# Performance work log

Measured on AMD Instinct MI355X. Metric: run time of the kernel, lower is better.

## Reference

```python
import jax, jax.numpy as jnp
import numpy as np
from jax import lax

INPUT_DIM = 2048
OUTPUT_DIM = 2048
BATCH = 256
T = 20.0
DT = 0.5
TAU_M = 20.0
TAU_S = 5.0
STEPS = int(T / DT)  # 40


def setup_inputs() -> dict:
    key = jax.random.key(0)
    k1, k2 = jax.random.split(key)
    # spike times on the t = i*dt grid (exactly representable in fp32)
    steps_idx = jax.random.randint(k1, (BATCH, INPUT_DIM), 0, STEPS)
    inp = steps_idx.astype(jnp.float32) * DT
    # nn.init.normal_(weight, mean=0.1, std=0.1)
    weight = 0.1 + 0.1 * jax.random.normal(k2, (OUTPUT_DIM, INPUT_DIM), dtype=jnp.float32)
    return {"input": inp, "weight": weight}


def _manual_forward(inp, weight):
    B = inp.shape[0]
    O = weight.shape[0]
    V0 = jnp.zeros((B, O), dtype=weight.dtype)
    I0 = jnp.zeros((B, O), dtype=weight.dtype)  # I[-1] row is zero at i=0

    def step(carry, i):
        V, I_prev = carry
        t = i.astype(weight.dtype) * DT
        V = V + (DT / TAU_M) * (I_prev - V)
        spikes_in = (inp == t).astype(weight.dtype)            # [B, in]
        I_i = (1.0 - DT / TAU_S) * I_prev + spikes_in @ weight.T  # [B, out]
        s = (V > 1.0).astype(weight.dtype)
        V = (1.0 - s) * V
        return (V, I_i), (I_i, s)

    (_, _), (I, post_spikes) = lax.scan(step, (V0, I0), jnp.arange(STEPS))
    # first spike time: idx decreasing so argmax picks earliest spiking step
    idx = jnp.arange(STEPS, 0, -1, dtype=weight.dtype)[:, None, None]
    first = jnp.argmax(idx * post_spikes, axis=0).astype(jnp.float32)
    # neurons with no spike (or spike at step 0, faithful to original) -> T
    first = jnp.where(first == 0.0, jnp.float32(T), first)
    return first, I, post_spikes


def reference(input, weight):
    first_post_spikes, _, _ = _manual_forward(input, weight)
    return first_post_spikes
```

## Files before the change

### kernel.cpp

```cpp
#include <hip/hip_runtime.h>


#define IN_DIM     2048
#define OUT_DIM    2048
#define BATCH      256
#define STEPS      40
#define NSLICE     32
#define ORD_STRIDE 2304

__global__ __launch_bounds__(256) void transpose_k(const float* __restrict__ W,
                                                   float* __restrict__ WT) {
    __shared__ float tile[64][65];
    const int bx = blockIdx.x;
    const int by = blockIdx.y;
    const int x  = threadIdx.x & 63;
    const int y4 = threadIdx.x >> 6;
#pragma unroll
    for (int i = 0; i < 16; ++i) {
        const int a = y4 * 16 + i;
        tile[a][x] = W[(size_t)(by * 64 + a) * IN_DIM + (bx * 64 + x)];
    }
    if (bx == 0 && y4 == 0)
        WT[(size_t)IN_DIM * OUT_DIM + by * 64 + x] = 0.0f;
    __syncthreads();
#pragma unroll
    for (int i = 0; i < 16; ++i) {
        const int r = y4 * 16 + i;
        WT[(size_t)(bx * 64 + r) * OUT_DIM + (by * 64 + x)] = tile[x][r];
    }
}

__global__ __launch_bounds__(256) void sort_k(const float* __restrict__ inp,
                                              int* __restrict__ ord,
                                              int* __restrict__ offs) {
    __shared__ int hist[256 * STEPS];
    __shared__ int tot[STEPS];
    __shared__ int binstart[STEPS + 1];
    const int b = blockIdx.x, t = threadIdx.x;
    for (int i = t; i < 256 * STEPS; i += 256) hist[i] = 0;
    __syncthreads();
    int ks[8];
#pragma unroll
    for (int i = 0; i < 8; ++i) {
        const float v = inp[b * IN_DIM + t * 8 + i];
        const int k = (int)(v * 2.0f);
        ks[i] = k;
        ++hist[t * STEPS + k];
    }
    __syncthreads();
    if (t < STEPS) {
        int run = 0;
        for (int tt = 0; tt < 256; ++tt) {
            const int c = hist[tt * STEPS + t];
            hist[tt * STEPS + t] = run;
            run += c;
        }
        tot[t] = run;
    }
    __syncthreads();
    if (t == 0) {
        int run = 0;
        for (int k = 0; k < STEPS; ++k) {
            binstart[k] = run;
            run += (tot[k] + 3) & ~3;
        }
        binstart[STEPS] = run;
    }
    __syncthreads();
    if (t <= STEPS) offs[b * (STEPS + 1) + t] = binstart[t];
#pragma unroll
    for (int i = 0; i < 8; ++i) {
        const int k = ks[i];
        const int pos = binstart[k] + hist[t * STEPS + k]++;
        ord[b * ORD_STRIDE + pos] = (t * 8 + i) * (OUT_DIM * 4);
    }
    if (t < STEPS) {
        const int beg = binstart[t] + tot[t];
        const int end = binstart[t] + ((tot[t] + 3) & ~3);
        for (int p = beg; p < end; ++p)
            ord[b * ORD_STRIDE + p] = IN_DIM * (OUT_DIM * 4);
    }
}

__global__ __launch_bounds__(64) void snn_k(const float* __restrict__ WT,
                                            const int* __restrict__ ord,
                                            const int* __restrict__ offs,
                                            float* __restrict__ out) {
    const int wid  = blockIdx.x;
    const int s    = wid & (NSLICE - 1);
    const int b    = wid >> 5;
    const int lane = threadIdx.x;
    const char* wb = (const char*)(WT + s * 64 + lane);
    const int* __restrict__ ob  = ord  + b * ORD_STRIDE;
    const int* __restrict__ off = offs + b * (STEPS + 1);

    float I = 0.f, V = 0.f;
    int   f = 0;
    int p = 0;
    for (int k = 0; k < STEPS; ++k) {
        const int e = off[k + 1];
        float a = 0.f;
        for (; p < e; p += 4) {
            const int4 jj = *(const int4*)(ob + p);
            a += *(const float*)(wb + jj.x);
            a += *(const float*)(wb + jj.y);
            a += *(const float*)(wb + jj.z);
            a += *(const float*)(wb + jj.w);
        }
        V += 0.025f * (I - V);
        I = 0.9f * I + a;
        if (V > 1.0f) { if (f == 0) f = k; V = 0.f; }
        if (__all(f != 0)) break;
    }
    out[(size_t)b * OUT_DIM + s * 64 + lane] = f ? (float)f : 20.0f;
}

extern "C" void kernel_launch(void* const* d_in, const int* in_sizes, int n_in,
                              void* d_out, int out_size, void* d_ws, size_t ws_size,
                              hipStream_t stream) {
    const float* inp = (const float*)d_in[0];
    const float* W   = (const float*)d_in[1];
    float* out = (float*)d_out;
    char*  ws  = (char*)d_ws;

    float* WT = (float*)ws;
    const size_t WT_BYTES = (size_t)(IN_DIM + 1) * OUT_DIM * sizeof(float);
    int* ord  = (int*)(ws + WT_BYTES);
    int* offs = (int*)(ws + WT_BYTES + (size_t)BATCH * ORD_STRIDE * sizeof(int));

    transpose_k<<<dim3(IN_DIM / 64, OUT_DIM / 64), 256, 0, stream>>>(W, WT);
    sort_k<<<BATCH, 256, 0, stream>>>(inp, ord, offs);
    snn_k<<<BATCH * NSLICE, 64, 0, stream>>>(WT, ord, offs, out);
}
```

Baseline: 53.65 us.

## Fuse transpose and sort into one prep kernel, parallelize histogram scan

Merges the weight transpose and the per-batch counting sort into a single launch, with the first 256 blocks doing the sort and the remaining blocks doing transpose tiles, sharing one shared-memory buffer. The sort's column-wise prefix scan, previously done serially by 40 threads over 256 entries each, is split into 160 threads that each handle a quarter chunk, followed by a chunk-offset pass and an in-place scan that folds in the bin start. This removes one kernel launch and shortens the serial scan, at the cost of a larger shared-memory footprint for the transpose blocks, which may lower their occupancy, and an extra barrier in the sort path.

```diff
diff --git a/kernel.cpp b/kernel.cpp
--- a/kernel.cpp
+++ b/kernel.cpp
@@ -8,35 +8,43 @@
 #define NSLICE     32
 #define ORD_STRIDE 2304
 
-__global__ __launch_bounds__(256) void transpose_k(const float* __restrict__ W,
-                                                   float* __restrict__ WT) {
-    __shared__ float tile[64][65];
-    const int bx = blockIdx.x;
-    const int by = blockIdx.y;
-    const int x  = threadIdx.x & 63;
-    const int y4 = threadIdx.x >> 6;
-#pragma unroll
-    for (int i = 0; i < 16; ++i) {
-        const int a = y4 * 16 + i;
-        tile[a][x] = W[(size_t)(by * 64 + a) * IN_DIM + (bx * 64 + x)];
-    }
-    if (bx == 0 && y4 == 0)
-        WT[(size_t)IN_DIM * OUT_DIM + by * 64 + x] = 0.0f;
-    __syncthreads();
-#pragma unroll
-    for (int i = 0; i < 16; ++i) {
-        const int r = y4 * 16 + i;
-        WT[(size_t)(bx * 64 + r) * OUT_DIM + (by * 64 + x)] = tile[x][r];
-    }
-}
-
-__global__ __launch_bounds__(256) void sort_k(const float* __restrict__ inp,
+__global__ __launch_bounds__(256) void prep_k(const float* __restrict__ W,
+                                              float* __restrict__ WT,
+                                              const float* __restrict__ inp,
                                               int* __restrict__ ord,
                                               int* __restrict__ offs) {
-    __shared__ int hist[256 * STEPS];
-    __shared__ int tot[STEPS];
-    __shared__ int binstart[STEPS + 1];
-    const int b = blockIdx.x, t = threadIdx.x;
+    __shared__ __align__(16) char smem[43008];
+    const int t = threadIdx.x;
+
+    if (blockIdx.x >= BATCH) {
+        float (*tile)[65] = (float (*)[65])smem;
+        const int id = blockIdx.x - BATCH;
+        const int bx = id & 31;
+        const int by = id >> 5;
+        const int x  = t & 63;
+        const int y4 = t >> 6;
+#pragma unroll
+        for (int i = 0; i < 16; ++i) {
+            const int a = y4 * 16 + i;
+            tile[a][x] = W[(size_t)(by * 64 + a) * IN_DIM + (bx * 64 + x)];
+        }
+        if (bx == 0 && y4 == 0)
+            WT[(size_t)IN_DIM * OUT_DIM + by * 64 + x] = 0.0f;
+        __syncthreads();
+#pragma unroll
+        for (int i = 0; i < 16; ++i) {
+            const int r = y4 * 16 + i;
+            WT[(size_t)(bx * 64 + r) * OUT_DIM + (by * 64 + x)] = tile[x][r];
+        }
+        return;
+    }
+
+    int* hist     = (int*)smem;
+    int* chunkcnt = (int*)(smem + 40960);
+    int* binstart = (int*)(smem + 40960 + 640);
+    int* tot      = (int*)(smem + 40960 + 640 + 164);
+    const int b = blockIdx.x;
+
     for (int i = t; i < 256 * STEPS; i += 256) hist[i] = 0;
     __syncthreads();
     int ks[8];
@@ -48,30 +56,51 @@
         ++hist[t * STEPS + k];
     }
     __syncthreads();
-    if (t < STEPS) {
+    if (t < STEPS * 4) {
+        const int k = t >> 2, q = t & 3;
         int run = 0;
-        for (int tt = 0; tt < 256; ++tt) {
-            const int c = hist[tt * STEPS + t];
-            hist[tt * STEPS + t] = run;
-            run += c;
+#pragma unroll
+        for (int i = 0; i < 64; i += 8) {
+            const int base = (q * 64 + i) * STEPS + k;
+            const int c0 = hist[base + 0 * STEPS], c1 = hist[base + 1 * STEPS];
+            const int c2 = hist[base + 2 * STEPS], c3 = hist[base + 3 * STEPS];
+            const int c4 = hist[base + 4 * STEPS], c5 = hist[base + 5 * STEPS];
+            const int c6 = hist[base + 6 * STEPS], c7 = hist[base + 7 * STEPS];
+            run += ((c0 + c1) + (c2 + c3)) + ((c4 + c5) + (c6 + c7));
         }
-        tot[t] = run;
+        chunkcnt[k * 4 + q] = run;
     }
     __syncthreads();
     if (t == 0) {
         int run = 0;
         for (int k = 0; k < STEPS; ++k) {
             binstart[k] = run;
-            run += (tot[k] + 3) & ~3;
+            const int tk = (chunkcnt[k * 4] + chunkcnt[k * 4 + 1]) +
+                           (chunkcnt[k * 4 + 2] + chunkcnt[k * 4 + 3]);
+            tot[k] = tk;
+            run += (tk + 3) & ~3;
         }
         binstart[STEPS] = run;
     }
     __syncthreads();
     if (t <= STEPS) offs[b * (STEPS + 1) + t] = binstart[t];
+    if (t < STEPS * 4) {
+        const int k = t >> 2, q = t & 3;
+        int run = binstart[k];
+        for (int qq = 0; qq < q; ++qq) run += chunkcnt[k * 4 + qq];
+#pragma unroll 8
+        for (int i = 0; i < 64; ++i) {
+            const int a = (q * 64 + i) * STEPS + k;
+            const int c = hist[a];
+            hist[a] = run;
+            run += c;
+        }
+    }
+    __syncthreads();
 #pragma unroll
     for (int i = 0; i < 8; ++i) {
         const int k = ks[i];
-        const int pos = binstart[k] + hist[t * STEPS + k]++;
+        const int pos = hist[t * STEPS + k]++;
         ord[b * ORD_STRIDE + pos] = (t * 8 + i) * (OUT_DIM * 4);
     }
     if (t < STEPS) {
@@ -128,7 +157,6 @@
     int* ord  = (int*)(ws + WT_BYTES);
     int* offs = (int*)(ws + WT_BYTES + (size_t)BATCH * ORD_STRIDE * sizeof(int));
 
-    transpose_k<<<dim3(IN_DIM / 64, OUT_DIM / 64), 256, 0, stream>>>(W, WT);
-    sort_k<<<BATCH, 256, 0, stream>>>(inp, ord, offs);
+    prep_k<<<BATCH + (IN_DIM / 64) * (OUT_DIM / 64), 256, 0, stream>>>(W, WT, inp, ord, offs);
     snn_k<<<BATCH * NSLICE, 64, 0, stream>>>(WT, ord, offs, out);
 }
```

After: 45.78 us. 14.7% less time.

## Fuse per-batch spike bucketing into the SNN kernel using shared memory

Applied to the files above, without the earlier changes.

The separate sort kernel is removed. Each 256-thread block of the SNN kernel now builds the per-step bucketed spike index list for its batch row in LDS and then runs four waves over different output slices. The global ord/offs round trip and one launch go away, the accumulation loop is unrolled to 8 gathers per iteration, and the transpose grid is linearized. In exchange, each batch row's sort is redone by 8 blocks, and the blocks use more LDS, which may limit occupancy.

```diff
diff --git a/kernel.cpp b/kernel.cpp
--- a/kernel.cpp
+++ b/kernel.cpp
@@ -1,18 +1,20 @@
 #include <hip/hip_runtime.h>
 
 
-#define IN_DIM     2048
-#define OUT_DIM    2048
-#define BATCH      256
-#define STEPS      40
-#define NSLICE     32
-#define ORD_STRIDE 2304
+#define IN_DIM   2048
+#define OUT_DIM  2048
+#define BATCH    256
+#define STEPS    40
+#define ROWBYTES (OUT_DIM * 4)
+#define HS       41
+#define ORD_CAP  2176
 
 __global__ __launch_bounds__(256) void transpose_k(const float* __restrict__ W,
                                                    float* __restrict__ WT) {
     __shared__ float tile[64][65];
-    const int bx = blockIdx.x;
-    const int by = blockIdx.y;
+    const int id = blockIdx.x;
+    const int by = id & 31;
+    const int bx = id >> 5;
     const int x  = threadIdx.x & 63;
     const int y4 = threadIdx.x >> 6;
 #pragma unroll
@@ -30,82 +32,104 @@
     }
 }
 
-__global__ __launch_bounds__(256) void sort_k(const float* __restrict__ inp,
-                                              int* __restrict__ ord,
-                                              int* __restrict__ offs) {
-    __shared__ int hist[256 * STEPS];
+__global__ __launch_bounds__(256) void snn_k(const float* __restrict__ WT,
+                                             const float* __restrict__ inp,
+                                             float* __restrict__ out) {
+    __shared__ __align__(16) int ordl[ORD_CAP];
+    __shared__ int hist[64 * HS];
+    __shared__ int bs[STEPS + 1];
     __shared__ int tot[STEPS];
-    __shared__ int binstart[STEPS + 1];
-    const int b = blockIdx.x, t = threadIdx.x;
-    for (int i = t; i < 256 * STEPS; i += 256) hist[i] = 0;
+
+    const int bid = blockIdx.x;
+    const int sg  = bid & 7;
+    const int b   = bid >> 3;
+    const int t   = threadIdx.x;
+
+    for (int i = t; i < 64 * HS; i += 256) hist[i] = 0;
     __syncthreads();
-    int ks[8];
+
+    int ks[32];
+    if (t < 64) {
+        const float* row = inp + (size_t)b * IN_DIM + t * 32;
 #pragma unroll
-    for (int i = 0; i < 8; ++i) {
-        const float v = inp[b * IN_DIM + t * 8 + i];
-        const int k = (int)(v * 2.0f);
-        ks[i] = k;
-        ++hist[t * STEPS + k];
+        for (int i = 0; i < 8; ++i) {
+            const float4 v = *(const float4*)(row + i * 4);
+            ks[i * 4 + 0] = (int)(v.x * 2.0f);
+            ks[i * 4 + 1] = (int)(v.y * 2.0f);
+            ks[i * 4 + 2] = (int)(v.z * 2.0f);
+            ks[i * 4 + 3] = (int)(v.w * 2.0f);
+        }
+#pragma unroll
+        for (int i = 0; i < 32; ++i) ++hist[t * HS + ks[i]];
     }
     __syncthreads();
+
     if (t < STEPS) {
         int run = 0;
-        for (int tt = 0; tt < 256; ++tt) {
-            const int c = hist[tt * STEPS + t];
-            hist[tt * STEPS + t] = run;
+        for (int tt = 0; tt < 64; ++tt) {
+            const int c = hist[tt * HS + t];
+            hist[tt * HS + t] = run;
             run += c;
         }
         tot[t] = run;
     }
     __syncthreads();
+
     if (t == 0) {
         int run = 0;
         for (int k = 0; k < STEPS; ++k) {
-            binstart[k] = run;
+            bs[k] = run;
             run += (tot[k] + 3) & ~3;
         }
-        binstart[STEPS] = run;
+        bs[STEPS] = run;
     }
     __syncthreads();
-    if (t <= STEPS) offs[b * (STEPS + 1) + t] = binstart[t];
+
+    if (t < 64) {
 #pragma unroll
-    for (int i = 0; i < 8; ++i) {
-        const int k = ks[i];
-        const int pos = binstart[k] + hist[t * STEPS + k]++;
-        ord[b * ORD_STRIDE + pos] = (t * 8 + i) * (OUT_DIM * 4);
+        for (int i = 0; i < 32; ++i) {
+            const int k = ks[i];
+            const int pos = bs[k] + hist[t * HS + k]++;
+            ordl[pos] = (t * 32 + i) * ROWBYTES;
+        }
+    } else if (t < 64 + STEPS) {
+        const int k = t - 64;
+        for (int p2 = bs[k] + tot[k]; p2 < bs[k + 1]; ++p2)
+            ordl[p2] = IN_DIM * ROWBYTES;
     }
-    if (t < STEPS) {
-        const int beg = binstart[t] + tot[t];
-        const int end = binstart[t] + ((tot[t] + 3) & ~3);
-        for (int p = beg; p < end; ++p)
-            ord[b * ORD_STRIDE + p] = IN_DIM * (OUT_DIM * 4);
-    }
-}
+    __syncthreads();
 
-__global__ __launch_bounds__(64) void snn_k(const float* __restrict__ WT,
-                                            const int* __restrict__ ord,
-                                            const int* __restrict__ offs,
-                                            float* __restrict__ out) {
-    const int wid  = blockIdx.x;
-    const int s    = wid & (NSLICE - 1);
-    const int b    = wid >> 5;
-    const int lane = threadIdx.x;
-    const char* wb = (const char*)(WT + s * 64 + lane);
-    const int* __restrict__ ob  = ord  + b * ORD_STRIDE;
-    const int* __restrict__ off = offs + b * (STEPS + 1);
+    const int wave = t >> 6, lane = t & 63;
+    const int s    = sg + wave * 8;
+    const char* wb = (const char*)WT + ((s * 64 + lane) << 2);
 
     float I = 0.f, V = 0.f;
     int   f = 0;
-    int p = 0;
+    int   p = 0;
     for (int k = 0; k < STEPS; ++k) {
-        const int e = off[k + 1];
+        const int e = bs[k + 1];
         float a = 0.f;
-        for (; p < e; p += 4) {
-            const int4 jj = *(const int4*)(ob + p);
-            a += *(const float*)(wb + jj.x);
-            a += *(const float*)(wb + jj.y);
-            a += *(const float*)(wb + jj.z);
-            a += *(const float*)(wb + jj.w);
+        for (; p + 8 <= e; p += 8) {
+            const int4 ja = *(const int4*)(ordl + p);
+            const int4 jb = *(const int4*)(ordl + p + 4);
+            const float w0 = *(const float*)(wb + ja.x);
+            const float w1 = *(const float*)(wb + ja.y);
+            const float w2 = *(const float*)(wb + ja.z);
+            const float w3 = *(const float*)(wb + ja.w);
+            const float w4 = *(const float*)(wb + jb.x);
+            const float w5 = *(const float*)(wb + jb.y);
+            const float w6 = *(const float*)(wb + jb.z);
+            const float w7 = *(const float*)(wb + jb.w);
+            a = (((((((((a + w0) + w1) + w2) + w3) + w4) + w5) + w6) + w7));
+        }
+        if (p < e) {
+            const int4 ja = *(const int4*)(ordl + p);
+            p += 4;
+            const float w0 = *(const float*)(wb + ja.x);
+            const float w1 = *(const float*)(wb + ja.y);
+            const float w2 = *(const float*)(wb + ja.z);
+            const float w3 = *(const float*)(wb + ja.w);
+            a = ((((a + w0) + w1) + w2) + w3);
         }
         V += 0.025f * (I - V);
         I = 0.9f * I + a;
@@ -121,14 +145,8 @@
     const float* inp = (const float*)d_in[0];
     const float* W   = (const float*)d_in[1];
     float* out = (float*)d_out;
-    char*  ws  = (char*)d_ws;
+    float* WT  = (float*)d_ws;
 
-    float* WT = (float*)ws;
-    const size_t WT_BYTES = (size_t)(IN_DIM + 1) * OUT_DIM * sizeof(float);
-    int* ord  = (int*)(ws + WT_BYTES);
-    int* offs = (int*)(ws + WT_BYTES + (size_t)BATCH * ORD_STRIDE * sizeof(int));
-
-    transpose_k<<<dim3(IN_DIM / 64, OUT_DIM / 64), 256, 0, stream>>>(W, WT);
-    sort_k<<<BATCH, 256, 0, stream>>>(inp, ord, offs);
-    snn_k<<<BATCH * NSLICE, 64, 0, stream>>>(WT, ord, offs, out);
+    transpose_k<<<(IN_DIM / 64) * (OUT_DIM / 64), 256, 0, stream>>>(W, WT);
+    snn_k<<<BATCH * 8, 256, 0, stream>>>(WT, inp, out);
 }
```

New measurement: 43.02 us, median of 2. 1.25x faster.
